# Performance work log

Hardware: AMD Instinct MI355X
Metric: run time of the kernel (lower is better)

The kernel has to match this reference:

```python
import jax, jax.numpy as jnp
import numpy as np

EPS = 1e-8  # torch F.cosine_similarity default eps


def setup_inputs() -> dict:
    key = jax.random.key(0)
    k1, k2 = jax.random.split(key)
    N, C = 131072, 1000
    logits = jax.random.normal(k1, (N, C), dtype=jnp.float32)
    labels = jax.random.randint(k2, (N,), 0, C, dtype=jnp.int64)
    return {"logits": logits, "labels": labels}


def reference(logits, labels):
    # cosine_similarity(logits, one_hot(labels)) == logits[i, labels[i]] / ||logits[i]||
    # (one-hot row has L2 norm 1). torch clamps sqrt(w1*w2) from below by eps.
    dot = jnp.take_along_axis(logits, labels[:, None], axis=1)[:, 0]  # [N]
    norm = jnp.sqrt(jnp.sum(logits * logits, axis=1))                 # [N], ||y||=1
    cos = dot / jnp.maximum(norm, EPS)
    return jnp.mean(1.0 - cos)
```

## Files before the change

### kernel.cpp

```cpp
#include <hip/hip_runtime.h>

#define WAVE 64
#define BLOCK 256
#define GRID 2048
#define EPSF 1e-8f

typedef float f4 __attribute__((ext_vector_type(4)));

__global__ __launch_bounds__(BLOCK) void cosine_loss_kernel(
    const float* __restrict__ logits,
    const int* __restrict__ labels,
    float* __restrict__ out,
    int N, int C, float inv_n)
{
    const int lane    = threadIdx.x & (WAVE - 1);
    const int wave_id = (blockIdx.x * BLOCK + threadIdx.x) >> 6;
    const int n_waves = (gridDim.x * BLOCK) >> 6;

    const int nvec = C >> 2;
    const int tail = nvec << 2;

    float local = 0.0f;

    int base = wave_id;

    for (; base + 3 * n_waves < N; base += 4 * n_waves) {
        const int r0 = base;
        const int r1 = base + n_waves;
        const int r2 = base + 2 * n_waves;
        const int r3 = base + 3 * n_waves;

        const f4* p0 = (const f4*)(logits + (size_t)r0 * (size_t)C);
        const f4* p1 = (const f4*)(logits + (size_t)r1 * (size_t)C);
        const f4* p2 = (const f4*)(logits + (size_t)r2 * (size_t)C);
        const f4* p3 = (const f4*)(logits + (size_t)r3 * (size_t)C);

        float dotk = 0.0f;
        if (lane < 4) {
            const int rk = base + lane * n_waves;
            const int lbl = labels[rk];
            dotk = logits[(size_t)rk * (size_t)C + (size_t)lbl];
        }

        float s0 = 0.0f, s1 = 0.0f, s2 = 0.0f, s3 = 0.0f;
        for (int c = lane; c < nvec; c += WAVE) {
            f4 a = __builtin_nontemporal_load(&p0[c]);
            f4 b = __builtin_nontemporal_load(&p1[c]);
            f4 d = __builtin_nontemporal_load(&p2[c]);
            f4 e = __builtin_nontemporal_load(&p3[c]);
            s0 = fmaf(a.x, a.x, fmaf(a.y, a.y, fmaf(a.z, a.z, fmaf(a.w, a.w, s0))));
            s1 = fmaf(b.x, b.x, fmaf(b.y, b.y, fmaf(b.z, b.z, fmaf(b.w, b.w, s1))));
            s2 = fmaf(d.x, d.x, fmaf(d.y, d.y, fmaf(d.z, d.z, fmaf(d.w, d.w, s2))));
            s3 = fmaf(e.x, e.x, fmaf(e.y, e.y, fmaf(e.z, e.z, fmaf(e.w, e.w, s3))));
        }
        for (int c = tail + lane; c < C; c += WAVE) {
            float v0 = logits[(size_t)r0 * C + c];
            float v1 = logits[(size_t)r1 * C + c];
            float v2 = logits[(size_t)r2 * C + c];
            float v3 = logits[(size_t)r3 * C + c];
            s0 = fmaf(v0, v0, s0);
            s1 = fmaf(v1, v1, s1);
            s2 = fmaf(v2, v2, s2);
            s3 = fmaf(v3, v3, s3);
        }

        #pragma unroll
        for (int off = 1; off < WAVE; off <<= 1) {
            s0 += __shfl_xor(s0, off, WAVE);
            s1 += __shfl_xor(s1, off, WAVE);
            s2 += __shfl_xor(s2, off, WAVE);
            s3 += __shfl_xor(s3, off, WAVE);
        }

        if (lane < 4) {
            const float ss = (lane == 0) ? s0 : (lane == 1) ? s1 : (lane == 2) ? s2 : s3;
            const float norm = sqrtf(ss);
            local += (1.0f - dotk / fmaxf(norm, EPSF)) * inv_n;
        }
    }

    for (; base < N; base += n_waves) {
        const f4* p = (const f4*)(logits + (size_t)base * (size_t)C);
        float dot = 0.0f;
        if (lane == 0) {
            const int lbl = labels[base];
            dot = logits[(size_t)base * (size_t)C + (size_t)lbl];
        }
        float ss = 0.0f;
        for (int c = lane; c < nvec; c += WAVE) {
            f4 v = __builtin_nontemporal_load(&p[c]);
            ss = fmaf(v.x, v.x, fmaf(v.y, v.y, fmaf(v.z, v.z, fmaf(v.w, v.w, ss))));
        }
        for (int c = tail + lane; c < C; c += WAVE) {
            float v = logits[(size_t)base * C + c];
            ss = fmaf(v, v, ss);
        }
        #pragma unroll
        for (int off = 32; off > 0; off >>= 1)
            ss += __shfl_down(ss, off, WAVE);
        if (lane == 0) {
            const float norm = sqrtf(ss);
            local += (1.0f - dot / fmaxf(norm, EPSF)) * inv_n;
        }
    }

    #pragma unroll
    for (int off = 32; off > 0; off >>= 1)
        local += __shfl_down(local, off, WAVE);

    __shared__ float sdata[BLOCK / WAVE];
    const int w = threadIdx.x >> 6;
    if (lane == 0) sdata[w] = local;
    __syncthreads();
    if (threadIdx.x == 0) {
        float s = 0.0f;
        #pragma unroll
        for (int i = 0; i < BLOCK / WAVE; ++i) s += sdata[i];
        atomicAdd(out, s);
    }
}

extern "C" void kernel_launch(void* const* d_in, const int* in_sizes, int n_in,
                              void* d_out, int out_size, void* d_ws, size_t ws_size,
                              hipStream_t stream) {
    const float* logits = (const float*)d_in[0];
    const int*   labels = (const int*)d_in[1];
    float*       out    = (float*)d_out;

    const int N = in_sizes[1];
    const int C = in_sizes[0] / N;
    const float inv_n = 1.0f / (float)N;

    hipMemsetAsync(d_out, 0, sizeof(float), stream);

    cosine_loss_kernel<<<GRID, BLOCK, 0, stream>>>(logits, labels, out, N, C, inv_n);
}
```

Baseline: 657.2 us.

## Prefetch label dots per lane and fully unroll row loads for small C

Restructures the row loop so each wave handles a group of up to 64 rows, with each lane prefetching its own row's label and target logit up front instead of doing a dependent gather inside every 4-row step. When C/4 is at most 256, the column loop is fully unrolled into 16 predicated vector loads issued together, which raises memory-level parallelism. Nontemporal loads are replaced by ordinary loads. The extra live registers may lower occupancy, and the strided row grouping changes the access pattern.

```diff
diff --git a/kernel.cpp b/kernel.cpp
--- a/kernel.cpp
+++ b/kernel.cpp
@@ -6,6 +6,10 @@
 #define EPSF 1e-8f
 
 typedef float f4 __attribute__((ext_vector_type(4)));
+
+__device__ __forceinline__ float sq4(f4 v, float acc) {
+    return fmaf(v.x, v.x, fmaf(v.y, v.y, fmaf(v.z, v.z, fmaf(v.w, v.w, acc))));
+}
 
 __global__ __launch_bounds__(BLOCK) void cosine_loss_kernel(
     const float* __restrict__ logits,
@@ -22,85 +26,152 @@
 
     float local = 0.0f;
 
-    int base = wave_id;
-
-    for (; base + 3 * n_waves < N; base += 4 * n_waves) {
-        const int r0 = base;
-        const int r1 = base + n_waves;
-        const int r2 = base + 2 * n_waves;
-        const int r3 = base + 3 * n_waves;
-
-        const f4* p0 = (const f4*)(logits + (size_t)r0 * (size_t)C);
-        const f4* p1 = (const f4*)(logits + (size_t)r1 * (size_t)C);
-        const f4* p2 = (const f4*)(logits + (size_t)r2 * (size_t)C);
-        const f4* p3 = (const f4*)(logits + (size_t)r3 * (size_t)C);
-
-        float dotk = 0.0f;
-        if (lane < 4) {
-            const int rk = base + lane * n_waves;
-            const int lbl = labels[rk];
-            dotk = logits[(size_t)rk * (size_t)C + (size_t)lbl];
+    for (int g0 = wave_id; g0 < N; g0 += (n_waves << 6)) {
+        const long long my_r = (long long)g0 + (long long)lane * (long long)n_waves;
+        float my_dot = 0.0f;
+        if (my_r < (long long)N) {
+            const int lbl = labels[my_r];
+            my_dot = logits[(size_t)my_r * (size_t)C + (size_t)lbl];
         }
 
-        float s0 = 0.0f, s1 = 0.0f, s2 = 0.0f, s3 = 0.0f;
-        for (int c = lane; c < nvec; c += WAVE) {
-            f4 a = __builtin_nontemporal_load(&p0[c]);
-            f4 b = __builtin_nontemporal_load(&p1[c]);
-            f4 d = __builtin_nontemporal_load(&p2[c]);
-            f4 e = __builtin_nontemporal_load(&p3[c]);
-            s0 = fmaf(a.x, a.x, fmaf(a.y, a.y, fmaf(a.z, a.z, fmaf(a.w, a.w, s0))));
-            s1 = fmaf(b.x, b.x, fmaf(b.y, b.y, fmaf(b.z, b.z, fmaf(b.w, b.w, s1))));
-            s2 = fmaf(d.x, d.x, fmaf(d.y, d.y, fmaf(d.z, d.z, fmaf(d.w, d.w, s2))));
-            s3 = fmaf(e.x, e.x, fmaf(e.y, e.y, fmaf(e.z, e.z, fmaf(e.w, e.w, s3))));
+        int nrows = (N - g0 + n_waves - 1) / n_waves;
+        if (nrows > 64) nrows = 64;
+
+        int k = 0;
+
+        if (nvec <= 256) {
+            const int c0 = lane;
+            const int c1 = lane + 64;
+            const int c2 = lane + 128;
+            const int c3 = lane + 192;
+            const bool k0 = c0 < nvec;
+            const bool k1 = c1 < nvec;
+            const bool k2 = c2 < nvec;
+            const bool k3 = c3 < nvec;
+            const f4 fz = {0.0f, 0.0f, 0.0f, 0.0f};
+
+            for (; k + 3 < nrows; k += 4) {
+                const size_t r0 = (size_t)g0 + (size_t)(k    ) * n_waves;
+                const size_t r1 = (size_t)g0 + (size_t)(k + 1) * n_waves;
+                const size_t r2 = (size_t)g0 + (size_t)(k + 2) * n_waves;
+                const size_t r3 = (size_t)g0 + (size_t)(k + 3) * n_waves;
+                const f4* p0 = (const f4*)(logits + r0 * (size_t)C);
+                const f4* p1 = (const f4*)(logits + r1 * (size_t)C);
+                const f4* p2 = (const f4*)(logits + r2 * (size_t)C);
+                const f4* p3 = (const f4*)(logits + r3 * (size_t)C);
+
+                f4 a0 = k0 ? p0[c0] : fz;
+                f4 a1 = k1 ? p0[c1] : fz;
+                f4 a2 = k2 ? p0[c2] : fz;
+                f4 a3 = k3 ? p0[c3] : fz;
+                f4 b0 = k0 ? p1[c0] : fz;
+                f4 b1 = k1 ? p1[c1] : fz;
+                f4 b2 = k2 ? p1[c2] : fz;
+                f4 b3 = k3 ? p1[c3] : fz;
+                f4 d0 = k0 ? p2[c0] : fz;
+                f4 d1 = k1 ? p2[c1] : fz;
+                f4 d2 = k2 ? p2[c2] : fz;
+                f4 d3 = k3 ? p2[c3] : fz;
+                f4 e0 = k0 ? p3[c0] : fz;
+                f4 e1 = k1 ? p3[c1] : fz;
+                f4 e2 = k2 ? p3[c2] : fz;
+                f4 e3 = k3 ? p3[c3] : fz;
+
+                float s0 = sq4(a3, sq4(a2, sq4(a1, sq4(a0, 0.0f))));
+                float s1 = sq4(b3, sq4(b2, sq4(b1, sq4(b0, 0.0f))));
+                float s2 = sq4(d3, sq4(d2, sq4(d1, sq4(d0, 0.0f))));
+                float s3 = sq4(e3, sq4(e2, sq4(e1, sq4(e0, 0.0f))));
+
+                for (int cc = tail + lane; cc < C; cc += WAVE) {
+                    float v0 = logits[r0 * (size_t)C + cc];
+                    float v1 = logits[r1 * (size_t)C + cc];
+                    float v2 = logits[r2 * (size_t)C + cc];
+                    float v3 = logits[r3 * (size_t)C + cc];
+                    s0 = fmaf(v0, v0, s0);
+                    s1 = fmaf(v1, v1, s1);
+                    s2 = fmaf(v2, v2, s2);
+                    s3 = fmaf(v3, v3, s3);
+                }
+
+                #pragma unroll
+                for (int off = 1; off < WAVE; off <<= 1) {
+                    s0 += __shfl_xor(s0, off, WAVE);
+                    s1 += __shfl_xor(s1, off, WAVE);
+                    s2 += __shfl_xor(s2, off, WAVE);
+                    s3 += __shfl_xor(s3, off, WAVE);
+                }
+
+                const int t = lane - k;
+                if (t >= 0 && t < 4) {
+                    const float ss = (t == 0) ? s0 : (t == 1) ? s1 : (t == 2) ? s2 : s3;
+                    const float norm = sqrtf(ss);
+                    local += (1.0f - my_dot / fmaxf(norm, EPSF)) * inv_n;
+                }
+            }
+        } else {
+            for (; k + 3 < nrows; k += 4) {
+                const size_t r0 = (size_t)g0 + (size_t)(k    ) * n_waves;
+                const size_t r1 = (size_t)g0 + (size_t)(k + 1) * n_waves;
+                const size_t r2 = (size_t)g0 + (size_t)(k + 2) * n_waves;
+                const size_t r3 = (size_t)g0 + (size_t)(k + 3) * n_waves;
+                const f4* p0 = (const f4*)(logits + r0 * (size_t)C);
+                const f4* p1 = (const f4*)(logits + r1 * (size_t)C);
+                const f4* p2 = (const f4*)(logits + r2 * (size_t)C);
+                const f4* p3 = (const f4*)(logits + r3 * (size_t)C);
+
+                float s0 = 0.0f, s1 = 0.0f, s2 = 0.0f, s3 = 0.0f;
+                for (int cc = lane; cc < nvec; cc += WAVE) {
+                    f4 a = p0[cc];
+                    f4 b = p1[cc];
+                    f4 d = p2[cc];
+                    f4 e = p3[cc];
+                    s0 = sq4(a, s0);
+                    s1 = sq4(b, s1);
+                    s2 = sq4(d, s2);
+                    s3 = sq4(e, s3);
+                }
+                for (int cc = tail + lane; cc < C; cc += WAVE) {
+                    float v0 = logits[r0 * (size_t)C + cc];
+                    float v1 = logits[r1 * (size_t)C + cc];
+                    float v2 = logits[r2 * (size_t)C + cc];
+                    float v3 = logits[r3 * (size_t)C + cc];
+                    s0 = fmaf(v0, v0, s0);
+                    s1 = fmaf(v1, v1, s1);
+                    s2 = fmaf(v2, v2, s2);
+                    s3 = fmaf(v3, v3, s3);
+                }
+                #pragma unroll
+                for (int off = 1; off < WAVE; off <<= 1) {
+                    s0 += __shfl_xor(s0, off, WAVE);
+                    s1 += __shfl_xor(s1, off, WAVE);
+                    s2 += __shfl_xor(s2, off, WAVE);
+                    s3 += __shfl_xor(s3, off, WAVE);
+                }
+                const int t = lane - k;
+                if (t >= 0 && t < 4) {
+                    const float ss = (t == 0) ? s0 : (t == 1) ? s1 : (t == 2) ? s2 : s3;
+                    const float norm = sqrtf(ss);
+                    local += (1.0f - my_dot / fmaxf(norm, EPSF)) * inv_n;
+                }
+            }
         }
-        for (int c = tail + lane; c < C; c += WAVE) {
-            float v0 = logits[(size_t)r0 * C + c];
-            float v1 = logits[(size_t)r1 * C + c];
-            float v2 = logits[(size_t)r2 * C + c];
-            float v3 = logits[(size_t)r3 * C + c];
-            s0 = fmaf(v0, v0, s0);
-            s1 = fmaf(v1, v1, s1);
-            s2 = fmaf(v2, v2, s2);
-            s3 = fmaf(v3, v3, s3);
-        }
-
-        #pragma unroll
-        for (int off = 1; off < WAVE; off <<= 1) {
-            s0 += __shfl_xor(s0, off, WAVE);
-            s1 += __shfl_xor(s1, off, WAVE);
-            s2 += __shfl_xor(s2, off, WAVE);
-            s3 += __shfl_xor(s3, off, WAVE);
-        }
-
-        if (lane < 4) {
-            const float ss = (lane == 0) ? s0 : (lane == 1) ? s1 : (lane == 2) ? s2 : s3;
-            const float norm = sqrtf(ss);
-            local += (1.0f - dotk / fmaxf(norm, EPSF)) * inv_n;
-        }
-    }
-
-    for (; base < N; base += n_waves) {
-        const f4* p = (const f4*)(logits + (size_t)base * (size_t)C);
-        float dot = 0.0f;
-        if (lane == 0) {
-            const int lbl = labels[base];
-            dot = logits[(size_t)base * (size_t)C + (size_t)lbl];
-        }
-        float ss = 0.0f;
-        for (int c = lane; c < nvec; c += WAVE) {
-            f4 v = __builtin_nontemporal_load(&p[c]);
-            ss = fmaf(v.x, v.x, fmaf(v.y, v.y, fmaf(v.z, v.z, fmaf(v.w, v.w, ss))));
-        }
-        for (int c = tail + lane; c < C; c += WAVE) {
-            float v = logits[(size_t)base * C + c];
-            ss = fmaf(v, v, ss);
-        }
-        #pragma unroll
-        for (int off = 32; off > 0; off >>= 1)
-            ss += __shfl_down(ss, off, WAVE);
-        if (lane == 0) {
-            const float norm = sqrtf(ss);
-            local += (1.0f - dot / fmaxf(norm, EPSF)) * inv_n;
+
+        for (; k < nrows; ++k) {
+            const size_t r = (size_t)g0 + (size_t)k * n_waves;
+            const f4* p = (const f4*)(logits + r * (size_t)C);
+            float ss = 0.0f;
+            for (int cc = lane; cc < nvec; cc += WAVE) ss = sq4(p[cc], ss);
+            for (int cc = tail + lane; cc < C; cc += WAVE) {
+                float v = logits[r * (size_t)C + cc];
+                ss = fmaf(v, v, ss);
+            }
+            #pragma unroll
+            for (int off = 1; off < WAVE; off <<= 1)
+                ss += __shfl_xor(ss, off, WAVE);
+            if (lane == k) {
+                const float norm = sqrtf(ss);
+                local += (1.0f - my_dot / fmaxf(norm, EPSF)) * inv_n;
+            }
         }
     }
 
```

After: 665.8 us. Within noise of the previous version (+1.3%).
